# Kernel optimization log

Measured on AMD Instinct MI355X. Metric: run time of the kernel, lower is better.

Reference implementation:

```python
import jax, jax.numpy as jnp
import numpy as np

D_IN = 1024
D_OUT = 1024

def setup_inputs() -> dict:
    key = jax.random.key(0)
    k1, k2 = jax.random.split(key)
    x = jax.random.normal(k1, (4, 2048, D_IN), dtype=jnp.float32)
    # Keras 'uniform' initializer: U(-0.05, 0.05); kernel has 4 slices, only 0..2 used
    kernel = jax.random.uniform(k2, (4, D_IN, D_OUT), dtype=jnp.float32, minval=-0.05, maxval=0.05)
    return {"x": x, "kernel": kernel}

def reference(x, kernel):
    # QKV projections: x [b, s, d] @ kernel[i] [d, e]
    WQ = jnp.einsum('bsd,de->bse', x, kernel[0])
    WK = jnp.einsum('bsd,de->bse', x, kernel[1])
    WV = jnp.einsum('bsd,de->bse', x, kernel[2])
    scale = 1.0 / jnp.sqrt(jnp.asarray(D_OUT, dtype=WQ.dtype))
    QK = jnp.einsum('bqe,bke->bqk', WQ, WK) * scale  # [b, s, s]
    A = jax.nn.softmax(QK, axis=-1)
    return jnp.einsum('bqk,bke->bqe', A, WV)  # [b, s, e]
```

## Files before the change

kernel.cpp:

```cpp
#include <hip/hip_runtime.h>
#include <hip/hip_bf16.h>
#include <cstdio>

typedef __bf16  bf16x8 __attribute__((ext_vector_type(8)));
typedef float   f32x4  __attribute__((ext_vector_type(4)));
typedef unsigned short u16;
typedef u16     u16x8  __attribute__((ext_vector_type(8)));
typedef u16     u16x4  __attribute__((ext_vector_type(4)));


__device__ __forceinline__ void gld_lds16(const void* g, void* l) {
  __builtin_amdgcn_global_load_lds(
      (const __attribute__((address_space(1))) unsigned int*)g,
      (__attribute__((address_space(3))) unsigned int*)l,
      16, 0, 0);
}

__device__ __forceinline__ u16 f2bf(float f) {
  union { float f; unsigned int u; } c{f};
  unsigned int u = c.u;
  u += 0x7fffu + ((u >> 16) & 1u);
  return (u16)(u >> 16);
}

__device__ __forceinline__ float bf2f(u16 h) {
  union { unsigned int u; float f; } c{(unsigned int)h << 16};
  return c.f;
}

enum { EPI_QKV = 0, EPI_QK = 1, EPI_PV = 2 };


__global__ __launch_bounds__(256) void prep_kernel(const float* __restrict__ x,
                                                   u16* __restrict__ xbf,
                                                   const float* __restrict__ w,
                                                   u16* __restrict__ wt) {
  __shared__ float tile[32][33];
  const int bid = blockIdx.x;
  if (bid < 4096) {
    const int i = (bid * 256 + threadIdx.x) * 8;
    float4 a = *(const float4*)(x + i);
    float4 b = *(const float4*)(x + i + 4);
    u16x8 r;
    r[0] = f2bf(a.x); r[1] = f2bf(a.y); r[2] = f2bf(a.z); r[3] = f2bf(a.w);
    r[4] = f2bf(b.x); r[5] = f2bf(b.y); r[6] = f2bf(b.z); r[7] = f2bf(b.w);
    *(u16x8*)(xbf + i) = r;
  } else {
    const int b2 = bid - 4096;
    const int s = b2 >> 10, r = b2 & 1023;
    const int e0 = (r & 31) * 32, d0 = (r >> 5) * 32;
    const int tx = threadIdx.x & 31, ty = threadIdx.x >> 5;
    const float* in = w + (size_t)s * 1048576;
#pragma unroll
    for (int j = 0; j < 4; ++j)
      tile[ty + j * 8][tx] = in[(size_t)(d0 + ty + j * 8) * 1024 + e0 + tx];
    __syncthreads();
    u16* o = wt + (size_t)s * 1048576;
#pragma unroll
    for (int j = 0; j < 4; ++j)
      o[(size_t)(e0 + ty + j * 8) * 1024 + d0 + tx] = f2bf(tile[tx][ty + j * 8]);
  }
}


template <int GX, int GY, int GZ>
__device__ __forceinline__ void xcd_swz(int& bx, int& by, int& bz) {
  constexpr int NWG = GX * GY * GZ;
  static_assert(NWG % 8 == 0, "grid must be divisible by 8");
  constexpr int Q8 = NWG / 8;
  int flat = blockIdx.x + GX * (blockIdx.y + GY * blockIdx.z);
  flat = (flat & 7) * Q8 + (flat >> 3);
  bx = flat % GX;
  by = (flat / GX) % GY;
  bz = flat / (GX * GY);
}


__device__ __forceinline__ void stage_half(const u16* __restrict__ g, int ld, int k0,
                                           u16* ldsb, int w, int l) {
  const int srow = l >> 3;
  const int scol = ((l & 7) ^ (srow & 7)) * 8;
#pragma unroll
  for (int q = 0; q < 2; ++q) {
    const int r = w * 16 + q * 8;
    gld_lds16(g + (long)(r + srow) * ld + k0 + scol, (void*)(ldsb + r * 64));
  }
}

template <int EPI, int GX, int GY, int GZ>
__global__ __launch_bounds__(512, 2)
void gemm256_bt(const u16* __restrict__ A, const u16* __restrict__ B,
                void* __restrict__ Cv, int K, int lda, int ldb, int ldc,
                long sA, long sB, long sC,
                u16* __restrict__ auxK, u16* __restrict__ auxV) {
  __shared__ __align__(16) u16 lds[65536];

  const int t = threadIdx.x;
  const int w = t >> 6, l = t & 63;
  const int wm = w >> 2, wn = w & 3;
  const int lr = l & 15, lq = l >> 4;
  const int rsw = l & 7;
  int bxs, bys, bz;
  xcd_swz<GX, GY, GZ>(bxs, bys, bz);
  const int m0 = bys * 256, n0 = bxs * 256;
  const u16* Ar = A + (long)bz * sA + (long)m0 * lda;
  const u16* Br = B + (long)bz * sB + (long)n0 * ldb;

  u16* curA = lds;
  u16* curB = lds + 16384;
  u16* nxtA = lds + 32768;
  u16* nxtB = lds + 49152;

  const int nt = K >> 6;

  f32x4 acc[8][4] = {};

  stage_half(Ar,             lda, 0, curA,        w, l);
  stage_half(Br,             ldb, 0, curB,        w, l);
  stage_half(Br + 128 * ldb, ldb, 0, curB + 8192, w, l);
  stage_half(Ar + 128 * lda, lda, 0, curA + 8192, w, l);
  asm volatile("s_waitcnt vmcnt(4)" ::: "memory");
  if (nt > 1) {
    stage_half(Ar,             lda, 64, nxtA,        w, l);
    stage_half(Br,             ldb, 64, nxtB,        w, l);
    stage_half(Br + 128 * ldb, ldb, 64, nxtB + 8192, w, l);
    asm volatile("s_waitcnt vmcnt(6)" ::: "memory");
  } else {
    asm volatile("s_waitcnt vmcnt(0)" ::: "memory");
  }
  __builtin_amdgcn_s_barrier();

  for (int tt = 0; tt < nt; ++tt) {
    const int kc = tt << 6;
    bf16x8 a0[4][2], a1[4][2], b0[2][2], b1[2][2];

#pragma unroll
    for (int mi = 0; mi < 4; ++mi)
#pragma unroll
      for (int j = 0; j < 2; ++j)
        a0[mi][j] = *(const bf16x8*)(curA + (wm * 128 + mi * 16 + lr) * 64 +
                                     (((j * 4 + lq) ^ rsw) * 8));
#pragma unroll
    for (int ni = 0; ni < 2; ++ni)
#pragma unroll
      for (int j = 0; j < 2; ++j)
        b0[ni][j] = *(const bf16x8*)(curB + (wn * 64 + ni * 16 + lr) * 64 +
                                     (((j * 4 + lq) ^ rsw) * 8));
    if (tt + 1 < nt)
      stage_half(Ar + 128 * lda, lda, kc + 64, nxtA + 8192, w, l);
    __builtin_amdgcn_s_barrier();
    asm volatile("s_waitcnt lgkmcnt(0)" ::: "memory");
    __builtin_amdgcn_sched_barrier(0);
    __builtin_amdgcn_s_setprio(1);
#pragma unroll
    for (int mi = 0; mi < 4; ++mi)
#pragma unroll
      for (int ni = 0; ni < 2; ++ni)
#pragma unroll
        for (int j = 0; j < 2; ++j)
          acc[mi][ni] = __builtin_amdgcn_mfma_f32_16x16x32_bf16(a0[mi][j], b0[ni][j], acc[mi][ni], 0, 0, 0);
    __builtin_amdgcn_s_setprio(0);
    __builtin_amdgcn_s_barrier();

#pragma unroll
    for (int ni = 0; ni < 2; ++ni)
#pragma unroll
      for (int j = 0; j < 2; ++j)
        b1[ni][j] = *(const bf16x8*)(curB + (wn * 64 + (ni + 2) * 16 + lr) * 64 +
                                     (((j * 4 + lq) ^ rsw) * 8));
    __builtin_amdgcn_s_barrier();
    asm volatile("s_waitcnt lgkmcnt(0)" ::: "memory");
    __builtin_amdgcn_sched_barrier(0);
    __builtin_amdgcn_s_setprio(1);
#pragma unroll
    for (int mi = 0; mi < 4; ++mi)
#pragma unroll
      for (int ni = 0; ni < 2; ++ni)
#pragma unroll
        for (int j = 0; j < 2; ++j)
          acc[mi][ni + 2] = __builtin_amdgcn_mfma_f32_16x16x32_bf16(a0[mi][j], b1[ni][j], acc[mi][ni + 2], 0, 0, 0);
    __builtin_amdgcn_s_setprio(0);
    __builtin_amdgcn_s_barrier();

#pragma unroll
    for (int mi = 0; mi < 4; ++mi)
#pragma unroll
      for (int j = 0; j < 2; ++j)
        a1[mi][j] = *(const bf16x8*)(curA + (wm * 128 + (mi + 4) * 16 + lr) * 64 +
                                     (((j * 4 + lq) ^ rsw) * 8));
    if (tt + 2 < nt)
      stage_half(Br, ldb, kc + 128, curB, w, l);
    __builtin_amdgcn_s_barrier();
    asm volatile("s_waitcnt lgkmcnt(0)" ::: "memory");
    __builtin_amdgcn_sched_barrier(0);
    __builtin_amdgcn_s_setprio(1);
#pragma unroll
    for (int mi = 0; mi < 4; ++mi)
#pragma unroll
      for (int ni = 0; ni < 2; ++ni)
#pragma unroll
        for (int j = 0; j < 2; ++j)
          acc[mi + 4][ni + 2] = __builtin_amdgcn_mfma_f32_16x16x32_bf16(a1[mi][j], b1[ni][j], acc[mi + 4][ni + 2], 0, 0, 0);
    __builtin_amdgcn_s_setprio(0);
    __builtin_amdgcn_s_barrier();

    if (tt + 2 < nt) {
      stage_half(Br + 128 * ldb, ldb, kc + 128, curB + 8192, w, l);
      stage_half(Ar,             lda, kc + 128, curA,        w, l);
    }
    __builtin_amdgcn_s_barrier();
    __builtin_amdgcn_sched_barrier(0);
    __builtin_amdgcn_s_setprio(1);
#pragma unroll
    for (int mi = 0; mi < 4; ++mi)
#pragma unroll
      for (int ni = 0; ni < 2; ++ni)
#pragma unroll
        for (int j = 0; j < 2; ++j)
          acc[mi + 4][ni] = __builtin_amdgcn_mfma_f32_16x16x32_bf16(a1[mi][j], b0[ni][j], acc[mi + 4][ni], 0, 0, 0);
    __builtin_amdgcn_s_setprio(0);
    if (tt + 2 < nt)      asm volatile("s_waitcnt vmcnt(6)" ::: "memory");
    else if (tt + 1 < nt) asm volatile("s_waitcnt vmcnt(0)" ::: "memory");
    __builtin_amdgcn_s_barrier();

    { u16* x_ = curA; curA = nxtA; nxtA = x_; }
    { u16* y_ = curB; curB = nxtB; nxtB = y_; }
  }

  if (EPI == EPI_QK) {
#pragma unroll
    for (int mi = 0; mi < 8; ++mi) {
#pragma unroll
      for (int i = 0; i < 4; ++i) {
        const int row = m0 + wm * 128 + mi * 16 + lq * 4 + i;
#pragma unroll
        for (int ni = 0; ni < 4; ++ni) {
          const int col = n0 + wn * 64 + ni * 16 + lr;
          const u16 h = f2bf(__expf(acc[mi][ni][i] * 0.03125f));
          ((u16*)Cv)[(long)bz * sC + (long)row * ldc + col] = h;
        }
      }
    }
    return;
  }

  u16* qkv_out = (n0 < 1024) ? (u16*)Cv : auxK;
  const int nl0 = n0 & 1023;
#pragma unroll
  for (int mi = 0; mi < 8; ++mi) {
#pragma unroll
    for (int i = 0; i < 4; ++i) {
      const int row = m0 + wm * 128 + mi * 16 + lq * 4 + i;
#pragma unroll
      for (int ni = 0; ni < 4; ++ni)
        qkv_out[(long)row * 1024 + nl0 + wn * 64 + ni * 16 + lr] = f2bf(acc[mi][ni][i]);
    }
  }
  (void)auxV;
}


template <int EPI, int GX, int GY, int GZ>
__global__ __launch_bounds__(256)
void gemm_bt(const u16* __restrict__ A, const u16* __restrict__ B,
             void* __restrict__ Cv, int K, int lda, int ldb, int ldc,
             long sA, long sB, long sC,
             u16* __restrict__ auxK, u16* __restrict__ auxV) {
  constexpr int LDS_U16 = (EPI == EPI_QKV) ? (128 * 136) : (128 * 128);
  __shared__ __align__(16) u16 lds[LDS_U16];
  u16* As = lds;
  u16* Bs = lds + 128 * 64;

  const int t = threadIdx.x;
  const int w = t >> 6, l = t & 63;
  int bxs, bys, bz;
  xcd_swz<GX, GY, GZ>(bxs, bys, bz);
  const u16* Ab = A + (long)bz * sA;
  const u16* Bb = B + (long)bz * sB;
  const int m0 = bys * 128, n0 = bxs * 128;
  const int wm = w & 1, wn = w >> 1;
  const int lr = l & 15, lq = l >> 4;
  const int srow = l >> 3;
  const int scol = ((l & 7) ^ ((l >> 3) & 7)) * 8;
  const int rsw = l & 7;

  f32x4 acc[4][4] = {};
  float rsp[4] = {0.f, 0.f, 0.f, 0.f};

  for (int k0 = 0; k0 < K; k0 += 64) {
    __syncthreads();
#pragma unroll
    for (int c = 0; c < 4; ++c) {
      const int rb = (w * 4 + c) * 8;
      gld_lds16(Ab + (long)(m0 + rb + srow) * lda + k0 + scol, (void*)(As + rb * 64));
      gld_lds16(Bb + (long)(n0 + rb + srow) * ldb + k0 + scol, (void*)(Bs + rb * 64));
    }
    __syncthreads();
#pragma unroll
    for (int j = 0; j < 2; ++j) {
      bf16x8 af[4], bfr[4];
#pragma unroll
      for (int i = 0; i < 4; ++i) {
        const int ch = ((j * 4 + lq) ^ rsw) * 8;
        af[i]  = *(const bf16x8*)(As + (wm * 64 + i * 16 + lr) * 64 + ch);
        bfr[i] = *(const bf16x8*)(Bs + (wn * 64 + i * 16 + lr) * 64 + ch);
      }
      if (EPI == EPI_PV) {
#pragma unroll
        for (int i = 0; i < 4; ++i)
#pragma unroll
          for (int e = 0; e < 8; ++e)
            rsp[i] += (float)af[i][e];
      }
#pragma unroll
      for (int mi = 0; mi < 4; ++mi)
#pragma unroll
        for (int ni = 0; ni < 4; ++ni)
          acc[mi][ni] = __builtin_amdgcn_mfma_f32_16x16x32_bf16(af[mi], bfr[ni], acc[mi][ni], 0, 0, 0);
    }
  }

  if (EPI == EPI_PV) {
#pragma unroll
    for (int i = 0; i < 4; ++i) {
      rsp[i] += __shfl_xor(rsp[i], 16, 64);
      rsp[i] += __shfl_xor(rsp[i], 32, 64);
    }
  }

  if (EPI == EPI_QKV && n0 >= 2048) {
    u16* tp = lds;
    __syncthreads();
#pragma unroll
    for (int mi = 0; mi < 4; ++mi) {
      const int row0 = wm * 64 + mi * 16 + lq * 4;
#pragma unroll
      for (int ni = 0; ni < 4; ++ni) {
        const int col = wn * 64 + ni * 16 + lr;
        u16x4 v4;
#pragma unroll
        for (int i = 0; i < 4; ++i) v4[i] = f2bf(acc[mi][ni][i]);
        *(u16x4*)(tp + col * 136 + row0) = v4;
      }
    }
    __syncthreads();
    const int e0 = n0 - 2048;
    const long bb = m0 >> 11;
    const int kbase = m0 & 2047;
    u16* vt_base = auxV + bb * 2097152;
#pragma unroll
    for (int q = 0; q < 8; ++q) {
      const int chunk = q * 256 + t;
      const int c = chunk >> 4, r0 = (chunk & 15) * 8;
      u16x8 v = *(const u16x8*)(tp + c * 136 + r0);
      *(u16x8*)(vt_base + (long)(e0 + c) * 2048 + kbase + r0) = v;
    }
    return;
  }

  u16* qkv_out = nullptr;
  int nl0 = 0;
  if (EPI == EPI_QKV) {
    qkv_out = (n0 < 1024) ? (u16*)Cv : auxK;
    nl0 = n0 & 1023;
  }

#pragma unroll
  for (int mi = 0; mi < 4; ++mi) {
#pragma unroll
    for (int i = 0; i < 4; ++i) {
      const int row = m0 + wm * 64 + mi * 16 + lq * 4 + i;
      float inv;
      if (EPI == EPI_PV) {
        const float rstot = __shfl(rsp[mi], lq * 4 + i, 64);
        inv = 1.0f / rstot;
      }
#pragma unroll
      for (int ni = 0; ni < 4; ++ni) {
        const float val = acc[mi][ni][i];
        const int col = n0 + wn * 64 + ni * 16 + lr;
        if (EPI == EPI_QKV) {
          qkv_out[(long)row * 1024 + nl0 + wn * 64 + ni * 16 + lr] = f2bf(val);
        } else if (EPI == EPI_QK) {
          const u16 h = f2bf(__expf(val * 0.03125f));
          ((u16*)Cv)[(long)bz * sC + (long)row * ldc + col] = h;
        } else {
          ((float*)Cv)[(long)bz * sC + (long)row * ldc + col] = val * inv;
        }
      }
    }
  }
}


extern "C" void kernel_launch(void* const* d_in, const int* in_sizes, int n_in,
                              void* d_out, int out_size, void* d_ws, size_t ws_size,
                              hipStream_t stream) {
  (void)in_sizes; (void)n_in; (void)out_size;
  const float* x    = (const float*)d_in[0];
  const float* kern = (const float*)d_in[1];
  float* out = (float*)d_out;
  char* ws = (char*)d_ws;
  const size_t MB = 1024 * 1024;
  u16*   xbf  = (u16*)(ws);
  u16*   WT   = (u16*)(ws + 16 * MB);
  u16*   Qc   = (u16*)(ws + 22 * MB);
  u16*   Kc   = (u16*)(ws + 38 * MB);
  u16*   VT   = (u16*)(ws + 54 * MB);
  u16*   SP   = (u16*)(ws + 70 * MB);
  if (ws_size < 102 * MB)
    fprintf(stderr, "WARNING: ws_size %zu too small\n", ws_size);

  prep_kernel<<<7168, 256, 0, stream>>>(x, xbf, kern, WT);
  gemm_bt<EPI_QKV, 24, 64, 1><<<dim3(24, 64, 1), 256, 0, stream>>>(
      xbf, WT, Qc, 1024, 1024, 1024, 1024, 0, 0, 0, Kc, VT);
  gemm256_bt<EPI_QK, 8, 8, 4><<<dim3(8, 8, 4), 512, 0, stream>>>(
      Qc, Kc, SP, 1024, 1024, 1024, 2048,
      2048L * 1024, 2048L * 1024, 2048L * 2048, nullptr, nullptr);
  gemm_bt<EPI_PV, 8, 16, 4><<<dim3(8, 16, 4), 256, 0, stream>>>(
      SP, VT, out, 2048, 2048, 2048, 1024,
      2048L * 2048, 1024L * 2048, 2048L * 1024, nullptr, nullptr);
}
```

Measured before the change: 233.7 us.

## Fuse four kernels into one persistent kernel with grid barriers

Replaces the four separate launches (prep, QKV GEMM, QK GEMM, PV GEMM) with a single persistent 256-block kernel. Software grid barriers built on an atomic counter separate the stages, and each 512-thread block acts as two 256-thread sub-blocks for the 128-tile stages. This removes launch overhead and inter-kernel gaps. In exchange it gives up the XCD-aware grid sizing of the separate launches, adds barrier spin costs, and makes the sub-blocks share __syncthreads, so their work is serialized. Grid barriers also assume all 256 blocks are co-resident.

```diff
diff --git a/kernel.cpp b/kernel.cpp
--- a/kernel.cpp
+++ b/kernel.cpp
@@ -8,6 +8,8 @@
 typedef u16     u16x8  __attribute__((ext_vector_type(8)));
 typedef u16     u16x4  __attribute__((ext_vector_type(4)));
 
+enum { EPI_QKV = 0, EPI_QK = 1, EPI_PV = 2 };
+
 
 __device__ __forceinline__ void gld_lds16(const void* g, void* l) {
   __builtin_amdgcn_global_load_lds(
@@ -23,56 +25,148 @@
   return (u16)(u >> 16);
 }
 
-__device__ __forceinline__ float bf2f(u16 h) {
-  union { unsigned int u; float f; } c{(unsigned int)h << 16};
-  return c.f;
-}
-
-enum { EPI_QKV = 0, EPI_QK = 1, EPI_PV = 2 };
-
-
-__global__ __launch_bounds__(256) void prep_kernel(const float* __restrict__ x,
-                                                   u16* __restrict__ xbf,
-                                                   const float* __restrict__ w,
-                                                   u16* __restrict__ wt) {
-  __shared__ float tile[32][33];
-  const int bid = blockIdx.x;
-  if (bid < 4096) {
-    const int i = (bid * 256 + threadIdx.x) * 8;
-    float4 a = *(const float4*)(x + i);
-    float4 b = *(const float4*)(x + i + 4);
-    u16x8 r;
-    r[0] = f2bf(a.x); r[1] = f2bf(a.y); r[2] = f2bf(a.z); r[3] = f2bf(a.w);
-    r[4] = f2bf(b.x); r[5] = f2bf(b.y); r[6] = f2bf(b.z); r[7] = f2bf(b.w);
-    *(u16x8*)(xbf + i) = r;
-  } else {
-    const int b2 = bid - 4096;
-    const int s = b2 >> 10, r = b2 & 1023;
-    const int e0 = (r & 31) * 32, d0 = (r >> 5) * 32;
-    const int tx = threadIdx.x & 31, ty = threadIdx.x >> 5;
-    const float* in = w + (size_t)s * 1048576;
-#pragma unroll
-    for (int j = 0; j < 4; ++j)
-      tile[ty + j * 8][tx] = in[(size_t)(d0 + ty + j * 8) * 1024 + e0 + tx];
+
+__device__ __forceinline__ void grid_bar(unsigned int* ctr) {
+  __threadfence();
+  __syncthreads();
+  if (threadIdx.x == 0) {
+    unsigned int old = __hip_atomic_fetch_add(ctr, 1u, __ATOMIC_ACQ_REL,
+                                              __HIP_MEMORY_SCOPE_AGENT);
+    unsigned int tgt = (old / 256u + 1u) * 256u;
+    while (__hip_atomic_load(ctr, __ATOMIC_ACQUIRE, __HIP_MEMORY_SCOPE_AGENT) < tgt)
+      __builtin_amdgcn_s_sleep(8);
+  }
+  __syncthreads();
+  __threadfence();
+}
+
+
+template <int EPI>
+__device__ void gemm128_tile(const u16* __restrict__ A, const u16* __restrict__ B,
+                             void* __restrict__ Cv, int K, int lda, int ldb, int ldc,
+                             long sA, long sB, long sC,
+                             u16* __restrict__ auxK, u16* __restrict__ auxV,
+                             u16* slds, int ts, int bxs, int bys, int bz) {
+  u16* As = slds;
+  u16* Bs = slds + 128 * 64;
+
+  const int w = ts >> 6, l = ts & 63;
+  const u16* Ab = A + (long)bz * sA;
+  const u16* Bb = B + (long)bz * sB;
+  const int m0 = bys * 128, n0 = bxs * 128;
+  const int wm = w & 1, wn = w >> 1;
+  const int lr = l & 15, lq = l >> 4;
+  const int srow = l >> 3;
+  const int scol = ((l & 7) ^ ((l >> 3) & 7)) * 8;
+  const int rsw = l & 7;
+
+  f32x4 acc[4][4] = {};
+  float rsp[4] = {0.f, 0.f, 0.f, 0.f};
+
+  for (int k0 = 0; k0 < K; k0 += 64) {
     __syncthreads();
-    u16* o = wt + (size_t)s * 1048576;
-#pragma unroll
-    for (int j = 0; j < 4; ++j)
-      o[(size_t)(e0 + ty + j * 8) * 1024 + d0 + tx] = f2bf(tile[tx][ty + j * 8]);
-  }
-}
-
-
-template <int GX, int GY, int GZ>
-__device__ __forceinline__ void xcd_swz(int& bx, int& by, int& bz) {
-  constexpr int NWG = GX * GY * GZ;
-  static_assert(NWG % 8 == 0, "grid must be divisible by 8");
-  constexpr int Q8 = NWG / 8;
-  int flat = blockIdx.x + GX * (blockIdx.y + GY * blockIdx.z);
-  flat = (flat & 7) * Q8 + (flat >> 3);
-  bx = flat % GX;
-  by = (flat / GX) % GY;
-  bz = flat / (GX * GY);
+#pragma unroll
+    for (int c = 0; c < 4; ++c) {
+      const int rb = (w * 4 + c) * 8;
+      gld_lds16(Ab + (long)(m0 + rb + srow) * lda + k0 + scol, (void*)(As + rb * 64));
+      gld_lds16(Bb + (long)(n0 + rb + srow) * ldb + k0 + scol, (void*)(Bs + rb * 64));
+    }
+    __syncthreads();
+#pragma unroll
+    for (int j = 0; j < 2; ++j) {
+      bf16x8 af[4], bfr[4];
+#pragma unroll
+      for (int i = 0; i < 4; ++i) {
+        const int ch = ((j * 4 + lq) ^ rsw) * 8;
+        af[i]  = *(const bf16x8*)(As + (wm * 64 + i * 16 + lr) * 64 + ch);
+        bfr[i] = *(const bf16x8*)(Bs + (wn * 64 + i * 16 + lr) * 64 + ch);
+      }
+      if (EPI == EPI_PV) {
+#pragma unroll
+        for (int i = 0; i < 4; ++i)
+#pragma unroll
+          for (int e = 0; e < 8; ++e)
+            rsp[i] += (float)af[i][e];
+      }
+#pragma unroll
+      for (int mi = 0; mi < 4; ++mi)
+#pragma unroll
+        for (int ni = 0; ni < 4; ++ni)
+          acc[mi][ni] = __builtin_amdgcn_mfma_f32_16x16x32_bf16(af[mi], bfr[ni], acc[mi][ni], 0, 0, 0);
+    }
+  }
+
+  if (EPI == EPI_PV) {
+#pragma unroll
+    for (int i = 0; i < 4; ++i) {
+      rsp[i] += __shfl_xor(rsp[i], 16, 64);
+      rsp[i] += __shfl_xor(rsp[i], 32, 64);
+    }
+  }
+
+  if (EPI == EPI_QKV && n0 >= 2048) {
+    u16* tp = slds;
+    __syncthreads();
+#pragma unroll
+    for (int mi = 0; mi < 4; ++mi) {
+      const int row0 = wm * 64 + mi * 16 + lq * 4;
+#pragma unroll
+      for (int ni = 0; ni < 4; ++ni) {
+        const int col = wn * 64 + ni * 16 + lr;
+        u16x4 v4;
+#pragma unroll
+        for (int i = 0; i < 4; ++i) v4[i] = f2bf(acc[mi][ni][i]);
+        *(u16x4*)(tp + col * 136 + row0) = v4;
+      }
+    }
+    __syncthreads();
+    const int e0 = n0 - 2048;
+    const long bb = m0 >> 11;
+    const int kbase = m0 & 2047;
+    u16* vt_base = auxV + bb * 2097152;
+#pragma unroll
+    for (int q = 0; q < 8; ++q) {
+      const int chunk = q * 256 + ts;
+      const int c = chunk >> 4, r0 = (chunk & 15) * 8;
+      u16x8 v = *(const u16x8*)(tp + c * 136 + r0);
+      *(u16x8*)(vt_base + (long)(e0 + c) * 2048 + kbase + r0) = v;
+    }
+    return;
+  }
+
+  if (EPI == EPI_QKV) __syncthreads();
+
+  u16* qkv_out = nullptr;
+  int nl0 = 0;
+  if (EPI == EPI_QKV) {
+    qkv_out = (n0 < 1024) ? (u16*)Cv : auxK;
+    nl0 = n0 & 1023;
+  }
+
+#pragma unroll
+  for (int mi = 0; mi < 4; ++mi) {
+#pragma unroll
+    for (int i = 0; i < 4; ++i) {
+      const int row = m0 + wm * 64 + mi * 16 + lq * 4 + i;
+      float inv;
+      if (EPI == EPI_PV) {
+        const float rstot = __shfl(rsp[mi], lq * 4 + i, 64);
+        inv = 1.0f / rstot;
+      }
+#pragma unroll
+      for (int ni = 0; ni < 4; ++ni) {
+        const float val = acc[mi][ni][i];
+        const int col = n0 + wn * 64 + ni * 16 + lr;
+        if (EPI == EPI_QKV) {
+          qkv_out[(long)row * 1024 + nl0 + wn * 64 + ni * 16 + lr] = f2bf(val);
+        } else {
+          ((float*)Cv)[(long)bz * sC + (long)row * ldc + col] = val * inv;
+        }
+      }
+    }
+  }
+
+  if (EPI == EPI_QKV) __syncthreads();
 }
 
 
@@ -87,22 +181,16 @@
   }
 }
 
-template <int EPI, int GX, int GY, int GZ>
-__global__ __launch_bounds__(512, 2)
-void gemm256_bt(const u16* __restrict__ A, const u16* __restrict__ B,
-                void* __restrict__ Cv, int K, int lda, int ldb, int ldc,
-                long sA, long sB, long sC,
-                u16* __restrict__ auxK, u16* __restrict__ auxV) {
-  __shared__ __align__(16) u16 lds[65536];
-
-  const int t = threadIdx.x;
+__device__ void gemm256_qk(const u16* __restrict__ A, const u16* __restrict__ B,
+                           u16* __restrict__ SPo, u16* lds, int t,
+                           int bxs, int bys, int bz) {
   const int w = t >> 6, l = t & 63;
   const int wm = w >> 2, wn = w & 3;
   const int lr = l & 15, lq = l >> 4;
   const int rsw = l & 7;
-  int bxs, bys, bz;
-  xcd_swz<GX, GY, GZ>(bxs, bys, bz);
   const int m0 = bys * 256, n0 = bxs * 256;
+  const int lda = 1024, ldb = 1024, ldc = 2048, K = 1024;
+  const long sA = 2048L * 1024, sB = 2048L * 1024, sC = 2048L * 2048;
   const u16* Ar = A + (long)bz * sA + (long)m0 * lda;
   const u16* Br = B + (long)bz * sB + (long)n0 * ldb;
 
@@ -227,168 +315,93 @@
     { u16* y_ = curB; curB = nxtB; nxtB = y_; }
   }
 
-  if (EPI == EPI_QK) {
-#pragma unroll
-    for (int mi = 0; mi < 8; ++mi) {
-#pragma unroll
-      for (int i = 0; i < 4; ++i) {
-        const int row = m0 + wm * 128 + mi * 16 + lq * 4 + i;
-#pragma unroll
-        for (int ni = 0; ni < 4; ++ni) {
-          const int col = n0 + wn * 64 + ni * 16 + lr;
-          const u16 h = f2bf(__expf(acc[mi][ni][i] * 0.03125f));
-          ((u16*)Cv)[(long)bz * sC + (long)row * ldc + col] = h;
-        }
-      }
-    }
-    return;
-  }
-
-  u16* qkv_out = (n0 < 1024) ? (u16*)Cv : auxK;
-  const int nl0 = n0 & 1023;
 #pragma unroll
   for (int mi = 0; mi < 8; ++mi) {
 #pragma unroll
     for (int i = 0; i < 4; ++i) {
       const int row = m0 + wm * 128 + mi * 16 + lq * 4 + i;
 #pragma unroll
-      for (int ni = 0; ni < 4; ++ni)
-        qkv_out[(long)row * 1024 + nl0 + wn * 64 + ni * 16 + lr] = f2bf(acc[mi][ni][i]);
-    }
-  }
-  (void)auxV;
-}
-
-
-template <int EPI, int GX, int GY, int GZ>
-__global__ __launch_bounds__(256)
-void gemm_bt(const u16* __restrict__ A, const u16* __restrict__ B,
-             void* __restrict__ Cv, int K, int lda, int ldb, int ldc,
-             long sA, long sB, long sC,
-             u16* __restrict__ auxK, u16* __restrict__ auxV) {
-  constexpr int LDS_U16 = (EPI == EPI_QKV) ? (128 * 136) : (128 * 128);
-  __shared__ __align__(16) u16 lds[LDS_U16];
-  u16* As = lds;
-  u16* Bs = lds + 128 * 64;
-
+      for (int ni = 0; ni < 4; ++ni) {
+        const int col = n0 + wn * 64 + ni * 16 + lr;
+        const u16 h = f2bf(__expf(acc[mi][ni][i] * 0.03125f));
+        SPo[(long)bz * sC + (long)row * ldc + col] = h;
+      }
+    }
+  }
+}
+
+
+__global__ __launch_bounds__(512, 2)
+void fused_attn(const float* __restrict__ x, const float* __restrict__ w,
+                u16* __restrict__ xbf, u16* __restrict__ wt,
+                u16* __restrict__ Qc, u16* __restrict__ Kc,
+                u16* __restrict__ VT, u16* __restrict__ SP,
+                float* __restrict__ out, unsigned int* __restrict__ ctr) {
+  __shared__ __align__(16) u16 lds[65536];
+  const int blk = blockIdx.x;
   const int t = threadIdx.x;
-  const int w = t >> 6, l = t & 63;
-  int bxs, bys, bz;
-  xcd_swz<GX, GY, GZ>(bxs, bys, bz);
-  const u16* Ab = A + (long)bz * sA;
-  const u16* Bb = B + (long)bz * sB;
-  const int m0 = bys * 128, n0 = bxs * 128;
-  const int wm = w & 1, wn = w >> 1;
-  const int lr = l & 15, lq = l >> 4;
-  const int srow = l >> 3;
-  const int scol = ((l & 7) ^ ((l >> 3) & 7)) * 8;
-  const int rsw = l & 7;
-
-  f32x4 acc[4][4] = {};
-  float rsp[4] = {0.f, 0.f, 0.f, 0.f};
-
-  for (int k0 = 0; k0 < K; k0 += 64) {
-    __syncthreads();
-#pragma unroll
-    for (int c = 0; c < 4; ++c) {
-      const int rb = (w * 4 + c) * 8;
-      gld_lds16(Ab + (long)(m0 + rb + srow) * lda + k0 + scol, (void*)(As + rb * 64));
-      gld_lds16(Bb + (long)(n0 + rb + srow) * ldb + k0 + scol, (void*)(Bs + rb * 64));
-    }
-    __syncthreads();
-#pragma unroll
-    for (int j = 0; j < 2; ++j) {
-      bf16x8 af[4], bfr[4];
-#pragma unroll
-      for (int i = 0; i < 4; ++i) {
-        const int ch = ((j * 4 + lq) ^ rsw) * 8;
-        af[i]  = *(const bf16x8*)(As + (wm * 64 + i * 16 + lr) * 64 + ch);
-        bfr[i] = *(const bf16x8*)(Bs + (wn * 64 + i * 16 + lr) * 64 + ch);
-      }
-      if (EPI == EPI_PV) {
-#pragma unroll
-        for (int i = 0; i < 4; ++i)
-#pragma unroll
-          for (int e = 0; e < 8; ++e)
-            rsp[i] += (float)af[i][e];
-      }
-#pragma unroll
-      for (int mi = 0; mi < 4; ++mi)
-#pragma unroll
-        for (int ni = 0; ni < 4; ++ni)
-          acc[mi][ni] = __builtin_amdgcn_mfma_f32_16x16x32_bf16(af[mi], bfr[ni], acc[mi][ni], 0, 0, 0);
-    }
-  }
-
-  if (EPI == EPI_PV) {
-#pragma unroll
-    for (int i = 0; i < 4; ++i) {
-      rsp[i] += __shfl_xor(rsp[i], 16, 64);
-      rsp[i] += __shfl_xor(rsp[i], 32, 64);
-    }
-  }
-
-  if (EPI == EPI_QKV && n0 >= 2048) {
-    u16* tp = lds;
-    __syncthreads();
-#pragma unroll
-    for (int mi = 0; mi < 4; ++mi) {
-      const int row0 = wm * 64 + mi * 16 + lq * 4;
-#pragma unroll
-      for (int ni = 0; ni < 4; ++ni) {
-        const int col = wn * 64 + ni * 16 + lr;
-        u16x4 v4;
-#pragma unroll
-        for (int i = 0; i < 4; ++i) v4[i] = f2bf(acc[mi][ni][i]);
-        *(u16x4*)(tp + col * 136 + row0) = v4;
-      }
-    }
-    __syncthreads();
-    const int e0 = n0 - 2048;
-    const long bb = m0 >> 11;
-    const int kbase = m0 & 2047;
-    u16* vt_base = auxV + bb * 2097152;
-#pragma unroll
-    for (int q = 0; q < 8; ++q) {
-      const int chunk = q * 256 + t;
-      const int c = chunk >> 4, r0 = (chunk & 15) * 8;
-      u16x8 v = *(const u16x8*)(tp + c * 136 + r0);
-      *(u16x8*)(vt_base + (long)(e0 + c) * 2048 + kbase + r0) = v;
-    }
-    return;
-  }
-
-  u16* qkv_out = nullptr;
-  int nl0 = 0;
-  if (EPI == EPI_QKV) {
-    qkv_out = (n0 < 1024) ? (u16*)Cv : auxK;
-    nl0 = n0 & 1023;
-  }
-
-#pragma unroll
-  for (int mi = 0; mi < 4; ++mi) {
-#pragma unroll
-    for (int i = 0; i < 4; ++i) {
-      const int row = m0 + wm * 64 + mi * 16 + lq * 4 + i;
-      float inv;
-      if (EPI == EPI_PV) {
-        const float rstot = __shfl(rsp[mi], lq * 4 + i, 64);
-        inv = 1.0f / rstot;
-      }
-#pragma unroll
-      for (int ni = 0; ni < 4; ++ni) {
-        const float val = acc[mi][ni][i];
-        const int col = n0 + wn * 64 + ni * 16 + lr;
-        if (EPI == EPI_QKV) {
-          qkv_out[(long)row * 1024 + nl0 + wn * 64 + ni * 16 + lr] = f2bf(val);
-        } else if (EPI == EPI_QK) {
-          const u16 h = f2bf(__expf(val * 0.03125f));
-          ((u16*)Cv)[(long)bz * sC + (long)row * ldc + col] = h;
-        } else {
-          ((float*)Cv)[(long)bz * sC + (long)row * ldc + col] = val * inv;
-        }
-      }
-    }
+  const int sb = t >> 8, ts = t & 255;
+  u16* slds = lds + sb * 17408;
+
+  {
+    const int vw = blk * 2 + sb;
+    float* tile = (float*)slds;
+#pragma unroll 1
+    for (int j = 0; j < 14; ++j) {
+      const int bid = vw * 14 + j;
+      if (bid < 4096) {
+        const int i = (bid * 256 + ts) * 8;
+        float4 a = *(const float4*)(x + i);
+        float4 b = *(const float4*)(x + i + 4);
+        u16x8 r;
+        r[0] = f2bf(a.x); r[1] = f2bf(a.y); r[2] = f2bf(a.z); r[3] = f2bf(a.w);
+        r[4] = f2bf(b.x); r[5] = f2bf(b.y); r[6] = f2bf(b.z); r[7] = f2bf(b.w);
+        *(u16x8*)(xbf + i) = r;
+        __syncthreads();
+        __syncthreads();
+      } else {
+        const int b2 = bid - 4096;
+        const int s = b2 >> 10, rr = b2 & 1023;
+        const int e0 = (rr & 31) * 32, d0 = (rr >> 5) * 32;
+        const int tx = ts & 31, ty = ts >> 5;
+        const float* in = w + (size_t)s * 1048576;
+#pragma unroll
+        for (int jj = 0; jj < 4; ++jj)
+          tile[(ty + jj * 8) * 33 + tx] = in[(size_t)(d0 + ty + jj * 8) * 1024 + e0 + tx];
+        __syncthreads();
+        u16* o = wt + (size_t)s * 1048576;
+#pragma unroll
+        for (int jj = 0; jj < 4; ++jj)
+          o[(size_t)(e0 + ty + jj * 8) * 1024 + d0 + tx] = f2bf(tile[tx * 33 + ty + jj * 8]);
+        __syncthreads();
+      }
+    }
+  }
+  grid_bar(ctr);
+
+  {
+#pragma unroll 1
+    for (int j = 0; j < 3; ++j) {
+      const int l1536 = (blk & 7) * 192 + (blk >> 3) * 6 + sb * 3 + j;
+      const int bxs = l1536 % 24, bys = l1536 / 24;
+      gemm128_tile<EPI_QKV>(xbf, wt, Qc, 1024, 1024, 1024, 1024, 0, 0, 0,
+                            Kc, VT, slds, ts, bxs, bys, 0);
+    }
+  }
+  grid_bar(ctr);
+
+  {
+    const int l256 = (blk & 7) * 32 + (blk >> 3);
+    gemm256_qk(Qc, Kc, SP, lds, t, l256 & 7, (l256 >> 3) & 7, l256 >> 6);
+  }
+  grid_bar(ctr);
+
+  {
+    const int l512 = (blk & 7) * 64 + (blk >> 3) * 2 + sb;
+    gemm128_tile<EPI_PV>(SP, VT, out, 2048, 2048, 2048, 1024,
+                         2048L * 2048, 1024L * 2048, 2048L * 1024,
+                         nullptr, nullptr, slds, ts,
+                         l512 & 7, (l512 >> 3) & 15, l512 >> 7);
   }
 }
 
@@ -408,16 +421,11 @@
   u16*   Kc   = (u16*)(ws + 38 * MB);
   u16*   VT   = (u16*)(ws + 54 * MB);
   u16*   SP   = (u16*)(ws + 70 * MB);
-  if (ws_size < 102 * MB)
+  unsigned int* CTR = (unsigned int*)(ws + 102 * MB);
+  if (ws_size < 102 * MB + 64)
     fprintf(stderr, "WARNING: ws_size %zu too small\n", ws_size);
 
-  prep_kernel<<<7168, 256, 0, stream>>>(x, xbf, kern, WT);
-  gemm_bt<EPI_QKV, 24, 64, 1><<<dim3(24, 64, 1), 256, 0, stream>>>(
-      xbf, WT, Qc, 1024, 1024, 1024, 1024, 0, 0, 0, Kc, VT);
-  gemm256_bt<EPI_QK, 8, 8, 4><<<dim3(8, 8, 4), 512, 0, stream>>>(
-      Qc, Kc, SP, 1024, 1024, 1024, 2048,
-      2048L * 1024, 2048L * 1024, 2048L * 2048, nullptr, nullptr);
-  gemm_bt<EPI_PV, 8, 16, 4><<<dim3(8, 16, 4), 256, 0, stream>>>(
-      SP, VT, out, 2048, 2048, 2048, 1024,
-      2048L * 2048, 1024L * 2048, 2048L * 1024, nullptr, nullptr);
-}
+  hipMemsetAsync(CTR, 0, 4, stream);
+  fused_attn<<<dim3(256), dim3(512), 0, stream>>>(
+      x, kern, xbf, WT, Qc, Kc, VT, SP, out, CTR);
+}
```

After: 669.5 us. 186% more time.
